# Performance work log

Hardware: AMD Instinct MI355X
Metric: run time of the kernel (lower is better)

The kernel has to match this reference:

```python
import jax, jax.numpy as jnp
import numpy as np

N_NODES = 100000
N_EDGES = 1600000
N_GRAPHS = 512
NUM_REL = 3


def setup_inputs() -> dict:
    key = jax.random.key(0)
    ks = jax.random.split(key, 16)
    shape_idx = jax.random.randint(ks[0], (N_NODES,), 0, 16)
    color_idx = jax.random.randint(ks[1], (N_NODES,), 0, 8)
    node_feats = jnp.stack([shape_idx, color_idx], axis=1)  # [N,2] int
    edge_index = jax.random.randint(ks[2], (2, N_EDGES), 0, N_NODES)
    edge_type = jax.random.randint(ks[3], (N_EDGES,), 0, NUM_REL)
    batch = jnp.sort(jax.random.randint(ks[4], (N_NODES,), 0, N_GRAPHS))
    s = lambda k, sh: jax.random.normal(k, sh, dtype=jnp.float32) * 0.05
    return {
        'node_feats': node_feats,
        'edge_index': edge_index,
        'edge_type': edge_type,
        'batch': batch,
        'shape_emb': s(ks[5], (16, 8)),
        'color_emb': s(ks[6], (8, 8)),
        'pre_w': s(ks[7], (16, 32)),
        'pre_b': jnp.zeros((32,), jnp.float32),
        'root1': s(ks[8], (32, 64)),
        'rel1': s(ks[9], (NUM_REL, 32, 64)),
        'bias1': jnp.zeros((64,), jnp.float32),
        'root2': s(ks[10], (64, 64)),
        'rel2': s(ks[11], (NUM_REL, 64, 64)),
        'bias2': jnp.zeros((64,), jnp.float32),
        'cls_w': s(ks[12], (64, 10)),
        'cls_b': jnp.zeros((10,), jnp.float32),
    }


def rgcn_conv(x, edge_index, edge_type, root, rel_w, bias):
    # PyG RGCNConv: out_i = x_i @ root + sum_r mean_{j in N_r(i)} x_j @ W_r + bias
    src, dst = edge_index[0], edge_index[1]
    out = x @ root + bias
    xs = x[src]  # [E, in] gathered source features
    for r in range(NUM_REL):
        m = (edge_type == r).astype(x.dtype)  # [E]
        msg = (xs @ rel_w[r]) * m[:, None]  # [E, out]
        agg = jax.ops.segment_sum(msg, dst, num_segments=N_NODES)
        cnt = jax.ops.segment_sum(m, dst, num_segments=N_NODES)
        out = out + agg / jnp.maximum(cnt, 1.0)[:, None]
    return out


def reference(node_feats, edge_index, edge_type, batch, shape_emb, color_emb,
              pre_w, pre_b, root1, rel1, bias1, root2, rel2, bias2, cls_w, cls_b):
    x = jnp.concatenate([shape_emb[node_feats[:, 0]], color_emb[node_feats[:, 1]]], axis=1)  # [N,16]
    x = jax.nn.relu(x @ pre_w + pre_b)  # [N,32]
    x = jax.nn.relu(rgcn_conv(x, edge_index, edge_type, root1, rel1, bias1))  # [N,64]
    x = jax.nn.relu(rgcn_conv(x, edge_index, edge_type, root2, rel2, bias2))  # [N,64]
    # global_mean_pool over graph ids
    s = jax.ops.segment_sum(x, batch, num_segments=N_GRAPHS)
    c = jax.ops.segment_sum(jnp.ones((x.shape[0],), x.dtype), batch, num_segments=N_GRAPHS)
    pooled = s / jnp.maximum(c, 1.0)[:, None]  # [G,64]
    return pooled @ cls_w + cls_b  # [G,num_classes]
```

## Files before the change

kernel.cpp:

```cpp
#include <hip/hip_runtime.h>

#define NN 100000
#define NE 1600000
#define NG 512

#define BSH 9
#define NB 196
#define EPB 8192
#define NAB ((NE + EPB - 1) / EPB)
#define CAP 9216

__global__ __launch_bounds__(256) void k_embed(
    const int* __restrict__ nf, const float* __restrict__ semb,
    const float* __restrict__ cemb, const float* __restrict__ pw,
    const float* __restrict__ pb, float* __restrict__ x1)
{
  int gid = blockIdx.x * 256 + threadIdx.x;
  bool valid = gid < NN;
  int i = valid ? gid : NN - 1;
  int sf = nf[2 * i], cf = nf[2 * i + 1];
  float x0[16];
#pragma unroll
  for (int k = 0; k < 8; ++k) x0[k] = semb[sf * 8 + k];
#pragma unroll
  for (int k = 0; k < 8; ++k) x0[8 + k] = cemb[cf * 8 + k];
  float acc[32];
#pragma unroll
  for (int j = 0; j < 32; ++j) acc[j] = pb[j];
#pragma unroll
  for (int k = 0; k < 16; ++k) {
    float xv = x0[k];
#pragma unroll
    for (int j = 0; j < 32; ++j) acc[j] += xv * pw[k * 32 + j];
  }
  if (valid) {
    float4* o = (float4*)(x1 + (size_t)i * 32);
#pragma unroll
    for (int j4 = 0; j4 < 8; ++j4) {
      float4 v;
      v.x = fmaxf(acc[4 * j4 + 0], 0.f);
      v.y = fmaxf(acc[4 * j4 + 1], 0.f);
      v.z = fmaxf(acc[4 * j4 + 2], 0.f);
      v.w = fmaxf(acc[4 * j4 + 3], 0.f);
      o[j4] = v;
    }
  }
}


__global__ __launch_bounds__(256) void kA_count(
    const int* __restrict__ ei, int* __restrict__ bkt_cnt)
{
  __shared__ int lh[NB];
  for (int b = threadIdx.x; b < NB; b += 256) lh[b] = 0;
  __syncthreads();
  int base = blockIdx.x * EPB;
#pragma unroll
  for (int i = 0; i < EPB / 256; ++i) {
    int e = base + i * 256 + threadIdx.x;
    if (e < NE) atomicAdd(&lh[ei[NE + e] >> BSH], 1);
  }
  __syncthreads();
  for (int b = threadIdx.x; b < NB; b += 256)
    if (lh[b]) atomicAdd(&bkt_cnt[b], lh[b]);
}

__global__ __launch_bounds__(256) void kA_scan(
    const int* __restrict__ bkt_cnt, int* __restrict__ bkt_base,
    int* __restrict__ bkt_cur)
{
  __shared__ int sm[2][256];
  int t = threadIdx.x;
  int v = (t < NB) ? bkt_cnt[t] : 0;
  sm[0][t] = v;
  __syncthreads();
  int cur = 0;
#pragma unroll
  for (int off = 1; off < 256; off <<= 1) {
    int add = (t >= off) ? sm[cur][t - off] : 0;
    sm[cur ^ 1][t] = sm[cur][t] + add;
    __syncthreads();
    cur ^= 1;
  }
  if (t < NB) {
    int ex = sm[cur][t] - v;
    bkt_base[t] = ex;
    bkt_cur[t] = ex;
  }
  if (t == 0) bkt_base[NB] = NE;
}

__global__ __launch_bounds__(256) void kA_scatter(
    const int* __restrict__ ei, const int* __restrict__ et,
    int* __restrict__ bkt_cur, int* __restrict__ binned)
{
  __shared__ int packA[EPB];
  __shared__ unsigned char bktA[EPB];
  __shared__ int lh[NB], grun[NB], lcur[NB];
  for (int b = threadIdx.x; b < NB; b += 256) { lh[b] = 0; lcur[b] = 0; }
  __syncthreads();
  int base = blockIdx.x * EPB;
#pragma unroll
  for (int i = 0; i < EPB / 256; ++i) {
    int p = i * 256 + threadIdx.x;
    int e = base + p;
    if (e < NE) {
      int src = ei[e], dst = ei[NE + e], ty = et[e];
      int b = dst >> BSH;
      packA[p] = src | (ty << 17) | ((dst & 511) << 19);
      bktA[p] = (unsigned char)b;
      atomicAdd(&lh[b], 1);
    } else {
      bktA[p] = 255;
    }
  }
  __syncthreads();
  for (int b = threadIdx.x; b < NB; b += 256)
    grun[b] = lh[b] ? atomicAdd(&bkt_cur[b], lh[b]) : 0;
  __syncthreads();
#pragma unroll
  for (int i = 0; i < EPB / 256; ++i) {
    int p = i * 256 + threadIdx.x;
    int b = bktA[p];
    if (b != 255) {
      int off = atomicAdd(&lcur[b], 1);
      binned[grun[b] + off] = packA[p];
    }
  }
}

__global__ __launch_bounds__(512) void kB_build(
    const int* __restrict__ bkt_base, const int* __restrict__ binned,
    int* __restrict__ rs3, int* __restrict__ ep)
{
  __shared__ int stage[CAP];
  __shared__ int ldeg3[1536], lrs3[1536], lcur3[1536];
  __shared__ int sm[2][512];
  int b = blockIdx.x;
  int t = threadIdx.x;
  int p0 = bkt_base[b], p1 = bkt_base[b + 1];
  int cnt = p1 - p0;
  int nodes0 = b << BSH;
  int nnodes = NN - nodes0 < 512 ? NN - nodes0 : 512;
  ldeg3[t] = 0; ldeg3[t + 512] = 0; ldeg3[t + 1024] = 0;
  lcur3[t] = 0; lcur3[t + 512] = 0; lcur3[t + 1024] = 0;
  __syncthreads();
  for (int p = t; p < cnt; p += 512) {
    int pk = binned[p0 + p];
    if (p < CAP) stage[p] = pk;
    int key = ((pk >> 19) & 511) * 3 + ((pk >> 17) & 3);
    atomicAdd(&ldeg3[key], 1);
  }
  __syncthreads();
  int s0 = ldeg3[3 * t], s1 = ldeg3[3 * t + 1], s2 = ldeg3[3 * t + 2];
  int tot = s0 + s1 + s2;
  sm[0][t] = tot;
  __syncthreads();
  int cur = 0;
#pragma unroll
  for (int off = 1; off < 512; off <<= 1) {
    int add = (t >= off) ? sm[cur][t - off] : 0;
    sm[cur ^ 1][t] = sm[cur][t] + add;
    __syncthreads();
    cur ^= 1;
  }
  int ex = sm[cur][t] - tot;
  int r0 = p0 + ex, r1 = r0 + s0, r2 = r1 + s1;
  lrs3[3 * t] = r0;
  lrs3[3 * t + 1] = r1;
  lrs3[3 * t + 2] = r2;
  if (t < nnodes) {
    size_t base3 = (size_t)(nodes0 + t) * 3;
    rs3[base3 + 0] = r0;
    rs3[base3 + 1] = r1;
    rs3[base3 + 2] = r2;
  }
  if (b == NB - 1 && t == 0) rs3[(size_t)NN * 3] = NE;
  __syncthreads();
  for (int p = t; p < cnt; p += 512) {
    int pk = (p < CAP) ? stage[p] : binned[p0 + p];
    int key = ((pk >> 19) & 511) * 3 + ((pk >> 17) & 3);
    int off = atomicAdd(&lcur3[key], 1);
    ep[lrs3[key] + off] = pk & 0x1FFFF;
  }
}

template <int IN>
__global__ __launch_bounds__(512) void k_fused(
    const float* __restrict__ x, const int* __restrict__ rs3,
    const int* __restrict__ ep, const float* __restrict__ root,
    const float* __restrict__ rel, const float* __restrict__ bias,
    float* __restrict__ y)
{
  __shared__ float smem[3 * IN][65];
  const int tid = threadIdx.x;
  const int node0 = blockIdx.x * 64;
  const int wv = tid >> 6;
  const int lane = tid & 63;

  constexpr int DPW = 64 / IN;
  constexpr int F4 = IN / 4;
  constexpr int NPF = (64 * F4) / 512;

  {
    const int k = lane & (IN - 1);
    const int sub = (IN == 64) ? 0 : (lane >> 5);
    const float* xk = x + k;
    for (int it = 0; it < 64 / (8 * DPW); ++it) {
      int dl = it * 8 * DPW + wv * DPW + sub;
      int d = node0 + dl;
      if (d < NN) {
        int q0 = rs3[3 * d + 0];
        int q1 = rs3[3 * d + 1];
        int q2 = rs3[3 * d + 2];
        int q3 = rs3[3 * d + 3];
        float a0 = 0.f, a1 = 0.f, a2 = 0.f;
        int p = q0;
        for (; p + 4 <= q3; p += 4) {
          int e0 = ep[p + 0];
          int e1 = ep[p + 1];
          int e2 = ep[p + 2];
          int e3 = ep[p + 3];
          float v0 = xk[(size_t)e0 * IN];
          float v1 = xk[(size_t)e1 * IN];
          float v2 = xk[(size_t)e2 * IN];
          float v3 = xk[(size_t)e3 * IN];
          a0 += ((p + 0 < q1) ? v0 : 0.f) + ((p + 1 < q1) ? v1 : 0.f) +
                ((p + 2 < q1) ? v2 : 0.f) + ((p + 3 < q1) ? v3 : 0.f);
          a1 += ((p + 0 >= q1 && p + 0 < q2) ? v0 : 0.f) +
                ((p + 1 >= q1 && p + 1 < q2) ? v1 : 0.f) +
                ((p + 2 >= q1 && p + 2 < q2) ? v2 : 0.f) +
                ((p + 3 >= q1 && p + 3 < q2) ? v3 : 0.f);
          a2 += ((p + 0 >= q2) ? v0 : 0.f) + ((p + 1 >= q2) ? v1 : 0.f) +
                ((p + 2 >= q2) ? v2 : 0.f) + ((p + 3 >= q2) ? v3 : 0.f);
        }
        for (; p < q3; ++p) {
          float v = xk[(size_t)ep[p] * IN];
          a0 += (p < q1) ? v : 0.f;
          a1 += (p >= q1 && p < q2) ? v : 0.f;
          a2 += (p >= q2) ? v : 0.f;
        }
        int c0 = q1 - q0, c1 = q2 - q1, c2 = q3 - q2;
        smem[0 * IN + k][dl] = a0 / (float)(c0 > 0 ? c0 : 1);
        smem[1 * IN + k][dl] = a1 / (float)(c1 > 0 ? c1 : 1);
        smem[2 * IN + k][dl] = a2 / (float)(c2 > 0 ? c2 : 1);
      }
    }
  }
  __syncthreads();

  const int n = lane;
  const int j0 = __builtin_amdgcn_readfirstlane(wv * 8);

  float4 pf[NPF];
#pragma unroll
  for (int u = 0; u < NPF; ++u) {
    int idx = u * 512 + tid;
    int nn = idx / F4, c4 = idx % F4;
    int node = node0 + nn;
    pf[u] = make_float4(0.f, 0.f, 0.f, 0.f);
    if (node < NN) pf[u] = *(const float4*)(x + (size_t)node * IN + c4 * 4);
  }

  float acc[8];
#pragma unroll
  for (int j = 0; j < 8; ++j) acc[j] = bias[j0 + j];

  auto mm = [&](const float* __restrict__ W, int row0) {
#pragma unroll 4
    for (int k = 0; k < IN; ++k) {
      float sk = smem[row0 + k][n];
      const float* w = W + (size_t)k * 64 + j0;
#pragma unroll
      for (int j = 0; j < 8; ++j) acc[j] = fmaf(sk, w[j], acc[j]);
    }
  };

  mm(rel, 0);
  mm(rel + (size_t)IN * 64, IN);
  mm(rel + (size_t)2 * IN * 64, 2 * IN);
  __syncthreads();

#pragma unroll
  for (int u = 0; u < NPF; ++u) {
    int idx = u * 512 + tid;
    int nn = idx / F4, c4 = idx % F4;
    smem[c4 * 4 + 0][nn] = pf[u].x;
    smem[c4 * 4 + 1][nn] = pf[u].y;
    smem[c4 * 4 + 2][nn] = pf[u].z;
    smem[c4 * 4 + 3][nn] = pf[u].w;
  }
  __syncthreads();
  mm(root, 0);

  int node = node0 + n;
  if (node < NN) {
    float4* o = (float4*)(y + (size_t)node * 64 + j0);
    float4 v;
    v.x = fmaxf(acc[0], 0.f);
    v.y = fmaxf(acc[1], 0.f);
    v.z = fmaxf(acc[2], 0.f);
    v.w = fmaxf(acc[3], 0.f);
    o[0] = v;
    v.x = fmaxf(acc[4], 0.f);
    v.y = fmaxf(acc[5], 0.f);
    v.z = fmaxf(acc[6], 0.f);
    v.w = fmaxf(acc[7], 0.f);
    o[1] = v;
  }
}

__global__ __launch_bounds__(256) void k_pool(
    const float* __restrict__ x3, const int* __restrict__ batch,
    float* __restrict__ pooled, float* __restrict__ gcnt)
{
  int gwave = (blockIdx.x * 256 + threadIdx.x) >> 6;
  int lane = threadIdx.x & 63;
  int n0 = gwave * 64;
  if (n0 >= NN) return;
  int n1 = n0 + 64 < NN ? n0 + 64 : NN;
  int gcur = batch[n0];
  float acc = 0.f;
  int run = 0;
  for (int n = n0; n < n1; ++n) {
    int g = batch[n];
    if (g != gcur) {
      atomicAdd(&pooled[gcur * 64 + lane], acc);
      if (lane == 0) atomicAdd(&gcnt[gcur], (float)run);
      acc = 0.f; run = 0; gcur = g;
    }
    acc += x3[(size_t)n * 64 + lane];
    ++run;
  }
  atomicAdd(&pooled[gcur * 64 + lane], acc);
  if (lane == 0) atomicAdd(&gcnt[gcur], (float)run);
}

__global__ __launch_bounds__(256) void k_cls(
    const float* __restrict__ pooled, const float* __restrict__ gcnt,
    const float* __restrict__ cw, const float* __restrict__ cb, float* __restrict__ out)
{
  int t = blockIdx.x * 256 + threadIdx.x;
  if (t >= NG * 10) return;
  int g = t / 10, c = t % 10;
  float cf = fmaxf(gcnt[g], 1.f);
  float acc = cb[c];
#pragma unroll 8
  for (int k = 0; k < 64; ++k)
    acc += (pooled[g * 64 + k] / cf) * cw[k * 10 + c];
  out[t] = acc;
}

extern "C" void kernel_launch(void* const* d_in, const int* in_sizes, int n_in,
                              void* d_out, int out_size, void* d_ws, size_t ws_size,
                              hipStream_t stream)
{
  const int* nf = (const int*)d_in[0];
  const int* ei = (const int*)d_in[1];
  const int* et = (const int*)d_in[2];
  const int* batch = (const int*)d_in[3];
  const float* semb = (const float*)d_in[4];
  const float* cemb = (const float*)d_in[5];
  const float* pw = (const float*)d_in[6];
  const float* pb = (const float*)d_in[7];
  const float* root1 = (const float*)d_in[8];
  const float* rel1 = (const float*)d_in[9];
  const float* bias1 = (const float*)d_in[10];
  const float* root2 = (const float*)d_in[11];
  const float* rel2 = (const float*)d_in[12];
  const float* bias2 = (const float*)d_in[13];
  const float* cw = (const float*)d_in[14];
  const float* cb = (const float*)d_in[15];
  float* out = (float*)d_out;

  char* ws = (char*)d_ws;
  size_t off = 0;
  auto alloc = [&](size_t bytes) {
    char* p = ws + off;
    off += (bytes + 255) & ~(size_t)255;
    return p;
  };
  int* bkt_cnt = (int*)alloc((size_t)NB * 4);
  int* bkt_base = (int*)alloc((size_t)(NB + 1) * 4);
  int* bkt_cur = (int*)alloc((size_t)NB * 4);
  int* rs3 = (int*)alloc(((size_t)NN * 3 + 1) * 4);
  int* ep = (int*)alloc((size_t)NE * 4 + 256);
  int* binned = (int*)alloc((size_t)NE * 4);
  float* xA = (float*)alloc((size_t)NN * 64 * 4);
  float* xB = (float*)alloc((size_t)NN * 64 * 4);
  float* pooled = (float*)alloc((size_t)NG * 64 * 4);
  float* gcnt = (float*)alloc((size_t)NG * 4);
  (void)ws_size; (void)in_sizes; (void)n_in; (void)out_size;

  hipMemsetAsync(bkt_cnt, 0, (size_t)NB * 4, stream);
  k_embed<<<(NN + 255) / 256, 256, 0, stream>>>(nf, semb, cemb, pw, pb, xB);

  kA_count<<<NAB, 256, 0, stream>>>(ei, bkt_cnt);
  kA_scan<<<1, 256, 0, stream>>>(bkt_cnt, bkt_base, bkt_cur);
  kA_scatter<<<NAB, 256, 0, stream>>>(ei, et, bkt_cur, binned);
  kB_build<<<NB, 512, 0, stream>>>(bkt_base, binned, rs3, ep);

  int fgrid = (NN + 63) / 64;

  k_fused<32><<<fgrid, 512, 0, stream>>>(xB, rs3, ep, root1, rel1, bias1, xA);
  k_fused<64><<<fgrid, 512, 0, stream>>>(xA, rs3, ep, root2, rel2, bias2, xB);

  hipMemsetAsync(pooled, 0, (size_t)NG * 64 * 4, stream);
  hipMemsetAsync(gcnt, 0, (size_t)NG * 4, stream);
  int nwaves = (NN + 63) / 64;
  k_pool<<<(nwaves + 3) / 4, 256, 0, stream>>>(xB, batch, pooled, gcnt);
  k_cls<<<(NG * 10 + 255) / 256, 256, 0, stream>>>(pooled, gcnt, cw, cb, out);
}
```

Baseline: 328.6 us.

## Parallelize aggregation over block edges with float4 gathers and LDS atomics

```diff
diff --git a/kernel.cpp b/kernel.cpp
--- a/kernel.cpp
+++ b/kernel.cpp
@@ -181,7 +181,7 @@
     int pk = (p < CAP) ? stage[p] : binned[p0 + p];
     int key = ((pk >> 19) & 511) * 3 + ((pk >> 17) & 3);
     int off = atomicAdd(&lcur3[key], 1);
-    ep[lrs3[key] + off] = pk & 0x1FFFF;
+    ep[lrs3[key] + off] = (pk & 0x7FFFF) | (((pk >> 19) & 63) << 19);
   }
 }
 
@@ -193,64 +193,54 @@
     float* __restrict__ y)
 {
   __shared__ float smem[3 * IN][65];
+  __shared__ float icnt[64 * 3];
   const int tid = threadIdx.x;
   const int node0 = blockIdx.x * 64;
   const int wv = tid >> 6;
   const int lane = tid & 63;
 
-  constexpr int DPW = 64 / IN;
   constexpr int F4 = IN / 4;
   constexpr int NPF = (64 * F4) / 512;
+  constexpr int EPI = 64 / F4;
+
+  float* sf = &smem[0][0];
+  for (int idx = tid; idx < 3 * IN * 65; idx += 512) sf[idx] = 0.f;
+  if (tid < 192) {
+    int dl = tid / 3, r = tid - 3 * dl;
+    int d = node0 + dl;
+    float c = 1.f;
+    if (d < NN) {
+      int a = rs3[3 * d + r];
+      int b = rs3[3 * d + r + 1];
+      c = (float)(b - a > 0 ? b - a : 1);
+    }
+    icnt[dl * 3 + r] = 1.f / c;
+  }
+  const int nend = (node0 + 64 < NN) ? node0 + 64 : NN;
+  const int E0 = rs3[3 * node0];
+  const int E1 = rs3[3 * nend];
+  __syncthreads();
 
   {
-    const int k = lane & (IN - 1);
-    const int sub = (IN == 64) ? 0 : (lane >> 5);
-    const float* xk = x + k;
-    for (int it = 0; it < 64 / (8 * DPW); ++it) {
-      int dl = it * 8 * DPW + wv * DPW + sub;
-      int d = node0 + dl;
-      if (d < NN) {
-        int q0 = rs3[3 * d + 0];
-        int q1 = rs3[3 * d + 1];
-        int q2 = rs3[3 * d + 2];
-        int q3 = rs3[3 * d + 3];
-        float a0 = 0.f, a1 = 0.f, a2 = 0.f;
-        int p = q0;
-        for (; p + 4 <= q3; p += 4) {
-          int e0 = ep[p + 0];
-          int e1 = ep[p + 1];
-          int e2 = ep[p + 2];
-          int e3 = ep[p + 3];
-          float v0 = xk[(size_t)e0 * IN];
-          float v1 = xk[(size_t)e1 * IN];
-          float v2 = xk[(size_t)e2 * IN];
-          float v3 = xk[(size_t)e3 * IN];
-          a0 += ((p + 0 < q1) ? v0 : 0.f) + ((p + 1 < q1) ? v1 : 0.f) +
-                ((p + 2 < q1) ? v2 : 0.f) + ((p + 3 < q1) ? v3 : 0.f);
-          a1 += ((p + 0 >= q1 && p + 0 < q2) ? v0 : 0.f) +
-                ((p + 1 >= q1 && p + 1 < q2) ? v1 : 0.f) +
-                ((p + 2 >= q1 && p + 2 < q2) ? v2 : 0.f) +
-                ((p + 3 >= q1 && p + 3 < q2) ? v3 : 0.f);
-          a2 += ((p + 0 >= q2) ? v0 : 0.f) + ((p + 1 >= q2) ? v1 : 0.f) +
-                ((p + 2 >= q2) ? v2 : 0.f) + ((p + 3 >= q2) ? v3 : 0.f);
-        }
-        for (; p < q3; ++p) {
-          float v = xk[(size_t)ep[p] * IN];
-          a0 += (p < q1) ? v : 0.f;
-          a1 += (p >= q1 && p < q2) ? v : 0.f;
-          a2 += (p >= q2) ? v : 0.f;
-        }
-        int c0 = q1 - q0, c1 = q2 - q1, c2 = q3 - q2;
-        smem[0 * IN + k][dl] = a0 / (float)(c0 > 0 ? c0 : 1);
-        smem[1 * IN + k][dl] = a1 / (float)(c1 > 0 ? c1 : 1);
-        smem[2 * IN + k][dl] = a2 / (float)(c2 > 0 ? c2 : 1);
+    const int es = lane / F4;
+    const int k4 = lane % F4;
+    for (int p = E0 + wv * EPI; p < E1; p += 8 * EPI) {
+      int idx = p + es;
+      bool valid = idx < E1;
+      int e = ep[valid ? idx : E1 - 1];
+      int src = e & 0x1FFFF;
+      int r = (e >> 17) & 3;
+      int dl = (e >> 19) & 63;
+      float4 v = *(const float4*)(x + (size_t)src * IN + k4 * 4);
+      if (valid) {
+        float* base = &smem[r * IN + k4 * 4][dl];
+        atomicAdd(base, v.x);
+        atomicAdd(base + 65, v.y);
+        atomicAdd(base + 130, v.z);
+        atomicAdd(base + 195, v.w);
       }
     }
   }
-  __syncthreads();
-
-  const int n = lane;
-  const int j0 = __builtin_amdgcn_readfirstlane(wv * 8);
 
   float4 pf[NPF];
 #pragma unroll
@@ -261,6 +251,17 @@
     pf[u] = make_float4(0.f, 0.f, 0.f, 0.f);
     if (node < NN) pf[u] = *(const float4*)(x + (size_t)node * IN + c4 * 4);
   }
+  __syncthreads();
+
+  for (int idx = tid; idx < 3 * IN * 64; idx += 512) {
+    int row = idx >> 6;
+    int dl = idx & 63;
+    smem[row][dl] *= icnt[dl * 3 + row / IN];
+  }
+  __syncthreads();
+
+  const int n = lane;
+  const int j0 = __builtin_amdgcn_readfirstlane(wv * 8);
 
   float acc[8];
 #pragma unroll
```

New measurement: 1.033 ms. 214% more time.

## Gather neighbor features with float4 loads and split edges across lanes

Applied to the files above, without the earlier changes.

```diff
diff --git a/kernel.cpp b/kernel.cpp
--- a/kernel.cpp
+++ b/kernel.cpp
@@ -198,59 +198,78 @@
   const int wv = tid >> 6;
   const int lane = tid & 63;
 
-  constexpr int DPW = 64 / IN;
+  constexpr int LPE = IN / 4;
+  constexpr int DPW = (IN == 32) ? 2 : 1;
+  constexpr int SW = 64 / DPW;
+  constexpr int EPI = SW / LPE;
+  const int sub = (IN == 64) ? 0 : (lane >> 5);
+  const int sl = lane % SW;
+  const int k4 = sl % LPE;
+  const int es = sl / LPE;
+
+  for (int it = 0; it < 8 / DPW; ++it) {
+    int dl = wv * 8 + it * DPW + sub;
+    int d = node0 + dl;
+    int q0 = 0, q1 = 0, q2 = 0, q3 = 0;
+    if (d < NN) {
+      q0 = rs3[3 * d + 0];
+      q1 = rs3[3 * d + 1];
+      q2 = rs3[3 * d + 2];
+      q3 = rs3[3 * d + 3];
+    }
+    float4 a0 = make_float4(0.f, 0.f, 0.f, 0.f);
+    float4 a1 = make_float4(0.f, 0.f, 0.f, 0.f);
+    float4 a2 = make_float4(0.f, 0.f, 0.f, 0.f);
+#pragma unroll 2
+    for (int p = q0; p < q3; p += EPI) {
+      int idx = p + es;
+      bool val = idx < q3;
+      int e = ep[val ? idx : q3 - 1];
+      float4 v = *(const float4*)(x + (size_t)e * IN + k4 * 4);
+      float m0 = (val && idx < q1) ? 1.f : 0.f;
+      float m1 = (val && idx >= q1 && idx < q2) ? 1.f : 0.f;
+      float m2 = (val && idx >= q2) ? 1.f : 0.f;
+      a0.x = fmaf(m0, v.x, a0.x); a0.y = fmaf(m0, v.y, a0.y);
+      a0.z = fmaf(m0, v.z, a0.z); a0.w = fmaf(m0, v.w, a0.w);
+      a1.x = fmaf(m1, v.x, a1.x); a1.y = fmaf(m1, v.y, a1.y);
+      a1.z = fmaf(m1, v.z, a1.z); a1.w = fmaf(m1, v.w, a1.w);
+      a2.x = fmaf(m2, v.x, a2.x); a2.y = fmaf(m2, v.y, a2.y);
+      a2.z = fmaf(m2, v.z, a2.z); a2.w = fmaf(m2, v.w, a2.w);
+    }
+#pragma unroll
+    for (int off = LPE; off < SW; off <<= 1) {
+      a0.x += __shfl_xor(a0.x, off, 64); a0.y += __shfl_xor(a0.y, off, 64);
+      a0.z += __shfl_xor(a0.z, off, 64); a0.w += __shfl_xor(a0.w, off, 64);
+      a1.x += __shfl_xor(a1.x, off, 64); a1.y += __shfl_xor(a1.y, off, 64);
+      a1.z += __shfl_xor(a1.z, off, 64); a1.w += __shfl_xor(a1.w, off, 64);
+      a2.x += __shfl_xor(a2.x, off, 64); a2.y += __shfl_xor(a2.y, off, 64);
+      a2.z += __shfl_xor(a2.z, off, 64); a2.w += __shfl_xor(a2.w, off, 64);
+    }
+    if (es == 0) {
+      float c0 = (float)(q1 - q0 > 0 ? q1 - q0 : 1);
+      float c1 = (float)(q2 - q1 > 0 ? q2 - q1 : 1);
+      float c2 = (float)(q3 - q2 > 0 ? q3 - q2 : 1);
+      int r0 = k4 * 4;
+      smem[0 * IN + r0 + 0][dl] = a0.x / c0;
+      smem[0 * IN + r0 + 1][dl] = a0.y / c0;
+      smem[0 * IN + r0 + 2][dl] = a0.z / c0;
+      smem[0 * IN + r0 + 3][dl] = a0.w / c0;
+      smem[1 * IN + r0 + 0][dl] = a1.x / c1;
+      smem[1 * IN + r0 + 1][dl] = a1.y / c1;
+      smem[1 * IN + r0 + 2][dl] = a1.z / c1;
+      smem[1 * IN + r0 + 3][dl] = a1.w / c1;
+      smem[2 * IN + r0 + 0][dl] = a2.x / c2;
+      smem[2 * IN + r0 + 1][dl] = a2.y / c2;
+      smem[2 * IN + r0 + 2][dl] = a2.z / c2;
+      smem[2 * IN + r0 + 3][dl] = a2.w / c2;
+    }
+  }
+  __syncthreads();
+
+  const int n = lane;
+  const int j0 = __builtin_amdgcn_readfirstlane(wv * 8);
   constexpr int F4 = IN / 4;
   constexpr int NPF = (64 * F4) / 512;
-
-  {
-    const int k = lane & (IN - 1);
-    const int sub = (IN == 64) ? 0 : (lane >> 5);
-    const float* xk = x + k;
-    for (int it = 0; it < 64 / (8 * DPW); ++it) {
-      int dl = it * 8 * DPW + wv * DPW + sub;
-      int d = node0 + dl;
-      if (d < NN) {
-        int q0 = rs3[3 * d + 0];
-        int q1 = rs3[3 * d + 1];
-        int q2 = rs3[3 * d + 2];
-        int q3 = rs3[3 * d + 3];
-        float a0 = 0.f, a1 = 0.f, a2 = 0.f;
-        int p = q0;
-        for (; p + 4 <= q3; p += 4) {
-          int e0 = ep[p + 0];
-          int e1 = ep[p + 1];
-          int e2 = ep[p + 2];
-          int e3 = ep[p + 3];
-          float v0 = xk[(size_t)e0 * IN];
-          float v1 = xk[(size_t)e1 * IN];
-          float v2 = xk[(size_t)e2 * IN];
-          float v3 = xk[(size_t)e3 * IN];
-          a0 += ((p + 0 < q1) ? v0 : 0.f) + ((p + 1 < q1) ? v1 : 0.f) +
-                ((p + 2 < q1) ? v2 : 0.f) + ((p + 3 < q1) ? v3 : 0.f);
-          a1 += ((p + 0 >= q1 && p + 0 < q2) ? v0 : 0.f) +
-                ((p + 1 >= q1 && p + 1 < q2) ? v1 : 0.f) +
-                ((p + 2 >= q1 && p + 2 < q2) ? v2 : 0.f) +
-                ((p + 3 >= q1 && p + 3 < q2) ? v3 : 0.f);
-          a2 += ((p + 0 >= q2) ? v0 : 0.f) + ((p + 1 >= q2) ? v1 : 0.f) +
-                ((p + 2 >= q2) ? v2 : 0.f) + ((p + 3 >= q2) ? v3 : 0.f);
-        }
-        for (; p < q3; ++p) {
-          float v = xk[(size_t)ep[p] * IN];
-          a0 += (p < q1) ? v : 0.f;
-          a1 += (p >= q1 && p < q2) ? v : 0.f;
-          a2 += (p >= q2) ? v : 0.f;
-        }
-        int c0 = q1 - q0, c1 = q2 - q1, c2 = q3 - q2;
-        smem[0 * IN + k][dl] = a0 / (float)(c0 > 0 ? c0 : 1);
-        smem[1 * IN + k][dl] = a1 / (float)(c1 > 0 ? c1 : 1);
-        smem[2 * IN + k][dl] = a2 / (float)(c2 > 0 ? c2 : 1);
-      }
-    }
-  }
-  __syncthreads();
-
-  const int n = lane;
-  const int j0 = __builtin_amdgcn_readfirstlane(wv * 8);
 
   float4 pf[NPF];
 #pragma unroll
@@ -297,15 +316,11 @@
   if (node < NN) {
     float4* o = (float4*)(y + (size_t)node * 64 + j0);
     float4 v;
-    v.x = fmaxf(acc[0], 0.f);
-    v.y = fmaxf(acc[1], 0.f);
-    v.z = fmaxf(acc[2], 0.f);
-    v.w = fmaxf(acc[3], 0.f);
+    v.x = fmaxf(acc[0], 0.f); v.y = fmaxf(acc[1], 0.f);
+    v.z = fmaxf(acc[2], 0.f); v.w = fmaxf(acc[3], 0.f);
     o[0] = v;
-    v.x = fmaxf(acc[4], 0.f);
-    v.y = fmaxf(acc[5], 0.f);
-    v.z = fmaxf(acc[6], 0.f);
-    v.w = fmaxf(acc[7], 0.f);
+    v.x = fmaxf(acc[4], 0.f); v.y = fmaxf(acc[5], 0.f);
+    v.z = fmaxf(acc[6], 0.f); v.w = fmaxf(acc[7], 0.f);
     o[1] = v;
   }
 }
```

Result: faster. 289.0 us (-12.0%).
